# Performance work log

Measured on AMD Instinct MI355X. Metric: run time of the kernel, lower is better.

## Reference

```python
import jax, jax.numpy as jnp
import numpy as np

N_TIME = 512          # n_time_nodes
LATENT = 32           # latent_dim
HIDDEN = 64           # hidden_dim
N_MODES = 8           # r_fourier_modes
X_A0 = 0.3            # initial stoichiometry (anode)
CSANMAX = 28700.0     # max concentration scale
BASE_LOGIT = float(np.log(X_A0 / (1.0 - X_A0)))  # logit_from_fraction(x_a0)
FEAT_DIM = 1 + 2 * N_MODES   # [rho, cos(k*pi*rho), sin(k*pi*rho)]
IN_DIM = LATENT + FEAT_DIM
N_POINTS = 2_000_000


def setup_inputs() -> dict:
    key = jax.random.key(0)
    ks = jax.random.split(key, 8)
    time_idx = jax.random.randint(ks[0], (N_POINTS,), 0, N_TIME)
    rho = jax.random.uniform(ks[1], (N_POINTS,), dtype=jnp.float32)
    # trainable latent code per nonzero time node
    emb = jax.random.normal(ks[2], (N_TIME - 1, LATENT), dtype=jnp.float32) * 0.02
    # decoder_a: Linear(IN,HID)+SiLU, Linear(HID,HID)+SiLU, Linear(HID,1)
    W0 = jax.random.normal(ks[3], (IN_DIM, HIDDEN), dtype=jnp.float32) / np.sqrt(IN_DIM)
    b0 = jnp.zeros((HIDDEN,), jnp.float32)
    W1 = jax.random.normal(ks[4], (HIDDEN, HIDDEN), dtype=jnp.float32) / np.sqrt(HIDDEN)
    b1 = jnp.zeros((HIDDEN,), jnp.float32)
    Wout = jax.random.normal(ks[5], (HIDDEN, 1), dtype=jnp.float32) * 0.1
    bout = jnp.zeros((1,), jnp.float32)
    return {"time_idx": time_idx, "rho": rho, "emb": emb,
            "W0": W0, "b0": b0, "W1": W1, "b1": b1, "Wout": Wout, "bout": bout}


def _radius_features(rho):
    # [N] -> [N, 1 + 2*N_MODES]
    k = jnp.arange(1, N_MODES + 1, dtype=rho.dtype)
    ang = jnp.pi * rho[:, None] * k[None, :]
    return jnp.concatenate([rho[:, None], jnp.cos(ang), jnp.sin(ang)], axis=1)


def reference(time_idx, rho, emb, W0, b0, W1, b1, Wout, bout):
    # predicated version of the torch masked scatter: compute everywhere,
    # select initial-condition value where time_idx == 0
    idx = jnp.clip(time_idx - 1, 0, N_TIME - 2)       # safe gather index
    e = emb[idx]                                       # [N, LATENT]
    feat = _radius_features(rho)                       # [N, FEAT_DIM]
    h = jnp.concatenate([e, feat], axis=1)             # [N, IN_DIM]
    h = jax.nn.silu(h @ W0 + b0)
    h = jax.nn.silu(h @ W1 + b1)
    raw = (h @ Wout + bout)[:, 0]                      # [N]
    theta = jax.nn.sigmoid(raw + BASE_LOGIT)
    return jnp.where(time_idx == 0, X_A0 * CSANMAX, theta * CSANMAX)
```

## Files before the change

kernel.cpp:

```cpp
#include <hip/hip_runtime.h>
#include <stdint.h>


typedef _Float16 half8  __attribute__((ext_vector_type(8)));
typedef _Float16 half4v __attribute__((ext_vector_type(4)));
typedef _Float16 half2v __attribute__((ext_vector_type(2)));
typedef float f32x4 __attribute__((ext_vector_type(4)));

#define LOG2E 1.44269504088896340736f
#define NLN2  -0.6931471805599453f
#define CSCL  -1.44269504088896340736f
#define BASE_LOGIT -0.84729786038720367f
#define CSANMAX 28700.0f
#define IC_VAL 8610.0f

__device__ __forceinline__ float fast_exp2(float x) { return __builtin_amdgcn_exp2f(x); }
__device__ __forceinline__ float fast_rcp(float x)  { return __builtin_amdgcn_rcpf(x); }
__device__ __forceinline__ float sigf(float x)  { return fast_rcp(1.0f + fast_exp2(-LOG2E * x)); }
__device__ __forceinline__ void usilu2(float u0, float u1, float& p0, float& p1) {
  const float d0 = 1.0f + fast_exp2(u0);
  const float d1 = 1.0f + fast_exp2(u1);
  const float r  = fast_rcp(d0 * d1);
  p0 = u0 * d1 * r;
  p1 = u1 * d0 * r;
}
__device__ __forceinline__ half2v pkh(float a, float b) {
  return __builtin_bit_cast(half2v, __builtin_amdgcn_cvt_pkrtz(a, b));
}

union H8 { half8 v8; half2v v2[4]; };
union H4 { half4v v4; half2v v2[2]; };

template <int CTRL>
__device__ __forceinline__ float dpp_radd(float x) {
  int yi = __builtin_amdgcn_update_dpp(0, __builtin_bit_cast(int, x), CTRL, 0xF, 0xF, false);
  return x + __builtin_bit_cast(float, yi);
}
__device__ __forceinline__ float row_sum16(float x) {
  x = dpp_radd<0xB1>(x);
  x = dpp_radd<0x4E>(x);
  x = dpp_radd<0x141>(x);
  x = dpp_radd<0x140>(x);
  return x;
}

__global__ __launch_bounds__(256, 4) void mlp_kernel(
    const int* __restrict__ tix, const float* __restrict__ rho,
    const float* __restrict__ emb, const float* __restrict__ W0,
    const float* __restrict__ b0, const float* __restrict__ W1,
    const float* __restrict__ b1, const float* __restrict__ Wout,
    const float* __restrict__ bout, float* __restrict__ out, int ntiles)
{
  __shared__ __align__(16) union {
    _Float16 stage0[2][4][64][8];
    _Float16 H[4][16][72];
  } shA;
  __shared__ __align__(16) _Float16 Wlds1[2][4][64][8];

  const int tid  = threadIdx.x;
  const int wid  = tid >> 6;
  const int lane = tid & 63;
  const int m    = lane & 15;
  const int q    = lane >> 4;

  _Float16 (*Hb)[72] = shA.H[wid];

  if (wid == 0) {
#pragma unroll
    for (int t = 0; t < 4; ++t) {
#pragma unroll
      for (int s = 0; s < 2; ++s) {
        half8 f0, f1;
#pragma unroll
        for (int j = 0; j < 8; ++j) {
          const int k = s * 32 + q * 8 + j;
          const int n = t * 16 + m;
          float v0;
          if (k < 32) {
            v0 = W0[k * 64 + n];
          } else {
            const int kn = k - 32;
            v0 = (kn < 16) ? W0[(33 + kn) * 64 + n]
               : (kn == 16) ? W0[32 * 64 + n]
               : (kn == 17) ? b0[n] : 0.0f;
          }
          f0[j] = (_Float16)(CSCL * v0);
          f1[j] = (_Float16)W1[k * 64 + n];
        }
        *(half8*)&shA.stage0[s][t][lane][0] = f0;
        *(half8*)&Wlds1[s][t][lane][0] = f1;
      }
    }
  }

  float bvt[4];
  float woutm[4];
#pragma unroll
  for (int t = 0; t < 4; ++t) {
    bvt[t]   = CSCL * b1[t * 16 + m];
    woutm[t] = NLN2 * Wout[t * 16 + m];
  }
  const float boutBL = bout[0] + BASE_LOGIT;

  __syncthreads();

  half8 w0A[4], w0B[4];
#pragma unroll
  for (int t = 0; t < 4; ++t) {
    w0A[t] = *(const half8*)&shA.stage0[0][t][lane][0];
    w0B[t] = *(const half8*)&shA.stage0[1][t][lane][0];
  }

  __syncthreads();

  const half8* wb1 = (const half8*)&Wlds1[0][0][0][0];

  const f32x4 z = {0.0f, 0.0f, 0.0f, 0.0f};
  const int tstride = gridDim.x * 4;

  int tg = blockIdx.x * 4 + wid;
  if (tg >= ntiles) return;
  const int lim = ntiles - 1;

  int   t0 = tix[tg * 16 + m];
  float r0 = rho[tg * 16 + m];
  const int tg1 = min(tg + tstride, lim);
  int   t1 = tix[tg1 * 16 + m];
  float r1 = rho[tg1 * 16 + m];
  {
    const int idx0 = min(max(t0 - 1, 0), 510);
  }
  const int idx0 = min(max(t0 - 1, 0), 510);
  const float* er0 = emb + (size_t)idx0 * 32 + q * 8;
  f32x4 eC0 = *(const f32x4*)er0;
  f32x4 eC1 = *(const f32x4*)(er0 + 4);

  while (true) {
    const int tg2 = min(tg + 2 * tstride, lim);
    const int   t2 = tix[tg2 * 16 + m];
    const float r2 = rho[tg2 * 16 + m];
    const int idxN = min(max(t1 - 1, 0), 510);
    const float* ern = emb + (size_t)idxN * 32 + q * 8;
    const f32x4 eN0 = *(const f32x4*)ern;
    const f32x4 eN1 = *(const f32x4*)(ern + 4);

    const float rhp = r0;
    const float rev = 0.5f * rhp;
    const float c1  = __builtin_amdgcn_cosf(rev);
    const float s1f = __builtin_amdgcn_sinf(rev);
    const float tc  = 2.0f * c1;
    const float x1v = (q == 0) ? c1 : ((q == 1) ? s1f : 0.0f);
    const float x0v = (q == 0) ? 1.0f : 0.0f;
    const float x2v = tc * x1v - x0v;
    const float x3v = tc * x2v - x1v;
    const float x4v = tc * x3v - x2v;
    const float x5v = tc * x4v - x3v;
    const float x6v = tc * x5v - x4v;
    const float x7v = tc * x6v - x5v;
    const float x8v = tc * x7v - x6v;
    H8 X1;
    X1.v2[0] = (q == 2) ? pkh(rhp, 1.0f) : pkh(x1v, x2v);
    X1.v2[1] = pkh(x3v, x4v);
    X1.v2[2] = pkh(x5v, x6v);
    X1.v2[3] = pkh(x7v, x8v);
    H8 X0;
    X0.v2[0] = pkh(eC0[0], eC0[1]); X0.v2[1] = pkh(eC0[2], eC0[3]);
    X0.v2[2] = pkh(eC1[0], eC1[1]); X0.v2[3] = pkh(eC1[2], eC1[3]);

    f32x4 acc[4];
#pragma unroll
    for (int t = 0; t < 4; ++t) {
      f32x4 a = __builtin_amdgcn_mfma_f32_16x16x32_f16(w0A[t], X0.v8, z, 0, 0, 0);
      a = __builtin_amdgcn_mfma_f32_16x16x32_f16(w0B[t], X1.v8, a, 0, 0, 0);
      acc[t] = a;
    }

    int z0 = 0;
    asm volatile("" : "+v"(z0));
    half8 w1A[4], w1B[4];
#pragma unroll
    for (int t = 0; t < 4; ++t) {
      w1A[t] = wb1[z0 + t * 64 + lane];
      w1B[t] = wb1[z0 + (4 + t) * 64 + lane];
    }

#pragma unroll
    for (int t = 0; t < 4; ++t) {
      float p0, p1, p2, p3;
      usilu2(acc[t][0], acc[t][1], p0, p1);
      usilu2(acc[t][2], acc[t][3], p2, p3);
      H4 hh;
      hh.v2[0] = pkh(p0, p1);
      hh.v2[1] = pkh(p2, p3);
      *(half4v*)&Hb[m][t * 16 + q * 4] = hh.v4;
    }

    const half8 Y0 = *(const half8*)&Hb[m][q * 8];
    const half8 Y1 = *(const half8*)&Hb[m][32 + q * 8];
#pragma unroll
    for (int t = 0; t < 4; ++t) {
      f32x4 a = __builtin_amdgcn_mfma_f32_16x16x32_f16(Y0, w1A[t], z, 0, 0, 0);
      a = __builtin_amdgcn_mfma_f32_16x16x32_f16(Y1, w1B[t], a, 0, 0, 0);
      acc[t] = a;
    }
    float dot0 = 0.0f, dot1 = 0.0f, dot2 = 0.0f, dot3 = 0.0f;
#pragma unroll
    for (int t = 0; t < 4; ++t) {
      float p0, p1, p2, p3;
      usilu2(acc[t][0] + bvt[t], acc[t][1] + bvt[t], p0, p1);
      usilu2(acc[t][2] + bvt[t], acc[t][3] + bvt[t], p2, p3);
      dot0 = fmaf(p0, woutm[t], dot0);
      dot1 = fmaf(p1, woutm[t], dot1);
      dot2 = fmaf(p2, woutm[t], dot2);
      dot3 = fmaf(p3, woutm[t], dot3);
    }
    dot0 = row_sum16(dot0);
    dot1 = row_sum16(dot1);
    dot2 = row_sum16(dot2);
    dot3 = row_sum16(dot3);
    const float dsel = (m & 2) ? ((m & 1) ? dot3 : dot2) : ((m & 1) ? dot1 : dot0);
    const float dg = __shfl(dsel, (m >> 2) * 16 + (m & 3), 64);

    const float theta = sigf(dg + boutBL);
    const float val = (t0 == 0) ? IC_VAL : theta * CSANMAX;
    if (q == 0) out[tg * 16 + m] = val;

    const int tgn = tg + tstride;
    if (tgn >= ntiles) break;
    tg = tgn;
    t0 = t1; r0 = r1;
    t1 = t2; r1 = r2;
    eC0 = eN0; eC1 = eN1;
  }
}

extern "C" void kernel_launch(void* const* d_in, const int* in_sizes, int n_in,
                              void* d_out, int out_size, void* d_ws, size_t ws_size,
                              hipStream_t stream) {
  const int*   tix  = (const int*)d_in[0];
  const float* rho  = (const float*)d_in[1];
  const float* emb  = (const float*)d_in[2];
  const float* W0   = (const float*)d_in[3];
  const float* b0   = (const float*)d_in[4];
  const float* W1   = (const float*)d_in[5];
  const float* b1   = (const float*)d_in[6];
  const float* Wout = (const float*)d_in[7];
  const float* bout = (const float*)d_in[8];
  float* outp = (float*)d_out;

  const int n      = in_sizes[0];
  const int ntiles = n / 16;

  int grid = 2048;
  const int maxg = (ntiles + 3) / 4;
  if (grid > maxg) grid = maxg;
  mlp_kernel<<<dim3(grid), dim3(256), 0, stream>>>(
      tix, rho, emb, W0, b0, W1, b1, Wout, bout, outp, ntiles);
}
```

Baseline: 167.6 us.

## Keep W1 fragments in registers and transpose layer-2 MFMA for cheaper output reduction

```diff
diff --git a/kernel.cpp b/kernel.cpp
--- a/kernel.cpp
+++ b/kernel.cpp
@@ -31,19 +31,6 @@
 union H8 { half8 v8; half2v v2[4]; };
 union H4 { half4v v4; half2v v2[2]; };
 
-template <int CTRL>
-__device__ __forceinline__ float dpp_radd(float x) {
-  int yi = __builtin_amdgcn_update_dpp(0, __builtin_bit_cast(int, x), CTRL, 0xF, 0xF, false);
-  return x + __builtin_bit_cast(float, yi);
-}
-__device__ __forceinline__ float row_sum16(float x) {
-  x = dpp_radd<0xB1>(x);
-  x = dpp_radd<0x4E>(x);
-  x = dpp_radd<0x141>(x);
-  x = dpp_radd<0x140>(x);
-  return x;
-}
-
 __global__ __launch_bounds__(256, 4) void mlp_kernel(
     const int* __restrict__ tix, const float* __restrict__ rho,
     const float* __restrict__ emb, const float* __restrict__ W0,
@@ -52,10 +39,9 @@
     const float* __restrict__ bout, float* __restrict__ out, int ntiles)
 {
   __shared__ __align__(16) union {
-    _Float16 stage0[2][4][64][8];
+    _Float16 stage[2][2][4][64][8];
     _Float16 H[4][16][72];
   } shA;
-  __shared__ __align__(16) _Float16 Wlds1[2][4][64][8];
 
   const int tid  = threadIdx.x;
   const int wid  = tid >> 6;
@@ -87,33 +73,38 @@
           f0[j] = (_Float16)(CSCL * v0);
           f1[j] = (_Float16)W1[k * 64 + n];
         }
-        *(half8*)&shA.stage0[s][t][lane][0] = f0;
-        *(half8*)&Wlds1[s][t][lane][0] = f1;
+        *(half8*)&shA.stage[0][s][t][lane][0] = f0;
+        *(half8*)&shA.stage[1][s][t][lane][0] = f1;
       }
     }
   }
 
-  float bvt[4];
-  float woutm[4];
+  f32x4 bq1acc[4];
+  f32x4 woutq[4];
 #pragma unroll
   for (int t = 0; t < 4; ++t) {
-    bvt[t]   = CSCL * b1[t * 16 + m];
-    woutm[t] = NLN2 * Wout[t * 16 + m];
+    const f32x4 bv = *(const f32x4*)(b1 + t * 16 + q * 4);
+    const f32x4 wv = *(const f32x4*)(Wout + t * 16 + q * 4);
+#pragma unroll
+    for (int r = 0; r < 4; ++r) {
+      bq1acc[t][r] = CSCL * bv[r];
+      woutq[t][r]  = NLN2 * wv[r];
+    }
   }
   const float boutBL = bout[0] + BASE_LOGIT;
 
   __syncthreads();
 
-  half8 w0A[4], w0B[4];
+  half8 w0A[4], w0B[4], w1A[4], w1B[4];
 #pragma unroll
   for (int t = 0; t < 4; ++t) {
-    w0A[t] = *(const half8*)&shA.stage0[0][t][lane][0];
-    w0B[t] = *(const half8*)&shA.stage0[1][t][lane][0];
+    w0A[t] = *(const half8*)&shA.stage[0][0][t][lane][0];
+    w0B[t] = *(const half8*)&shA.stage[0][1][t][lane][0];
+    w1A[t] = *(const half8*)&shA.stage[1][0][t][lane][0];
+    w1B[t] = *(const half8*)&shA.stage[1][1][t][lane][0];
   }
 
   __syncthreads();
-
-  const half8* wb1 = (const half8*)&Wlds1[0][0][0][0];
 
   const f32x4 z = {0.0f, 0.0f, 0.0f, 0.0f};
   const int tstride = gridDim.x * 4;
@@ -127,9 +118,6 @@
   const int tg1 = min(tg + tstride, lim);
   int   t1 = tix[tg1 * 16 + m];
   float r1 = rho[tg1 * 16 + m];
-  {
-    const int idx0 = min(max(t0 - 1, 0), 510);
-  }
   const int idx0 = min(max(t0 - 1, 0), 510);
   const float* er0 = emb + (size_t)idx0 * 32 + q * 8;
   f32x4 eC0 = *(const f32x4*)er0;
@@ -174,16 +162,6 @@
       a = __builtin_amdgcn_mfma_f32_16x16x32_f16(w0B[t], X1.v8, a, 0, 0, 0);
       acc[t] = a;
     }
-
-    int z0 = 0;
-    asm volatile("" : "+v"(z0));
-    half8 w1A[4], w1B[4];
-#pragma unroll
-    for (int t = 0; t < 4; ++t) {
-      w1A[t] = wb1[z0 + t * 64 + lane];
-      w1B[t] = wb1[z0 + (4 + t) * 64 + lane];
-    }
-
 #pragma unroll
     for (int t = 0; t < 4; ++t) {
       float p0, p1, p2, p3;
@@ -199,29 +177,26 @@
     const half8 Y1 = *(const half8*)&Hb[m][32 + q * 8];
 #pragma unroll
     for (int t = 0; t < 4; ++t) {
-      f32x4 a = __builtin_amdgcn_mfma_f32_16x16x32_f16(Y0, w1A[t], z, 0, 0, 0);
-      a = __builtin_amdgcn_mfma_f32_16x16x32_f16(Y1, w1B[t], a, 0, 0, 0);
+      f32x4 a = __builtin_amdgcn_mfma_f32_16x16x32_f16(w1A[t], Y0, bq1acc[t], 0, 0, 0);
+      a = __builtin_amdgcn_mfma_f32_16x16x32_f16(w1B[t], Y1, a, 0, 0, 0);
       acc[t] = a;
     }
-    float dot0 = 0.0f, dot1 = 0.0f, dot2 = 0.0f, dot3 = 0.0f;
+    float dA = 0.0f, dB = 0.0f;
 #pragma unroll
     for (int t = 0; t < 4; ++t) {
       float p0, p1, p2, p3;
-      usilu2(acc[t][0] + bvt[t], acc[t][1] + bvt[t], p0, p1);
-      usilu2(acc[t][2] + bvt[t], acc[t][3] + bvt[t], p2, p3);
-      dot0 = fmaf(p0, woutm[t], dot0);
-      dot1 = fmaf(p1, woutm[t], dot1);
-      dot2 = fmaf(p2, woutm[t], dot2);
-      dot3 = fmaf(p3, woutm[t], dot3);
-    }
-    dot0 = row_sum16(dot0);
-    dot1 = row_sum16(dot1);
-    dot2 = row_sum16(dot2);
-    dot3 = row_sum16(dot3);
-    const float dsel = (m & 2) ? ((m & 1) ? dot3 : dot2) : ((m & 1) ? dot1 : dot0);
-    const float dg = __shfl(dsel, (m >> 2) * 16 + (m & 3), 64);
-
-    const float theta = sigf(dg + boutBL);
+      usilu2(acc[t][0], acc[t][1], p0, p1);
+      usilu2(acc[t][2], acc[t][3], p2, p3);
+      dA = fmaf(p0, woutq[t][0], dA);
+      dB = fmaf(p1, woutq[t][1], dB);
+      dA = fmaf(p2, woutq[t][2], dA);
+      dB = fmaf(p3, woutq[t][3], dB);
+    }
+    float dot = dA + dB;
+    dot += __shfl_xor(dot, 16, 64);
+    dot += __shfl_xor(dot, 32, 64);
+
+    const float theta = sigf(dot + boutBL);
     const float val = (t0 == 0) ? IC_VAL : theta * CSANMAX;
     if (q == 0) out[tg * 16 + m] = val;
 
@@ -251,7 +226,7 @@
   const int n      = in_sizes[0];
   const int ntiles = n / 16;
 
-  int grid = 2048;
+  int grid = 1024;
   const int maxg = (ntiles + 3) / 4;
   if (grid > maxg) grid = maxg;
   mlp_kernel<<<dim3(grid), dim3(256), 0, stream>>>(
```

Result: slower. 185.5 us (+10.7%).
